# Optimization experiments

Hardware: AMD Instinct MI355X
Metric: run time of the kernel (lower is better)

## Reference

```python
import jax, jax.numpy as jnp
import numpy as np

# ProbAttention (Yangskm/DroneMA-i-), eval mode (dropout=identity).
# Key facts from the source: mask_flag=False, scale=None -> `if self.scale` is
# False, so scores are NOT divided by sqrt(D). The _prob_QK sampling/topk result
# `u` and _get_initial_context are dead code w.r.t. the returned context, so the
# output is exactly dense softmax attention. Inputs are (B, L, H, D); the module
# transposes to (B, H, L, D) and transposes back at the end.

def setup_inputs() -> dict:
    key = jax.random.key(0)
    k1, k2, k3 = jax.random.split(key, 3)
    B, L, H, D = 4, 2048, 8, 64
    return {
        "queries": jax.random.normal(k1, (B, L, H, D), dtype=jnp.float32),
        "keys": jax.random.normal(k2, (B, L, H, D), dtype=jnp.float32),
        "values": jax.random.normal(k3, (B, L, H, D), dtype=jnp.float32),
    }

def reference(queries, keys, values):
    # (B, L, H, D) -> (B, H, L, D)
    q = jnp.swapaxes(queries, 1, 2)
    k = jnp.swapaxes(keys, 1, 2)
    v = jnp.swapaxes(values, 1, 2)
    # dense scores, NO 1/sqrt(D) scaling (scale=None in the original)
    scores = jnp.einsum("bhqd,bhkd->bhqk", q, k)
    attn = jax.nn.softmax(scores, axis=-1)
    ctx = jnp.einsum("bhqk,bhkd->bhqd", attn, v)
    # back to (B, L, H, D)
    return jnp.swapaxes(ctx, 1, 2)
```

## Files before the change

### kernel.cpp

```cpp
#include <hip/hip_runtime.h>
#include <hip/hip_bf16.h>


#define B_ 4
#define L_ 2048
#define H_ 8
#define D_ 64
#define RST_ 512
#define QW_ 32
#define QB_ 128
#define KT_ 64
#define NT_ (L_ / KT_)
#define RS_ 88
#define OTS_ 68
#define SCW_ 35
#define LOG2E_ 1.44269504088896f

#define SMEM_BYTES 35840

typedef _Float16 f16x8 __attribute__((ext_vector_type(8)));
typedef short    s16x4 __attribute__((ext_vector_type(4)));
typedef float    f32x4 __attribute__((ext_vector_type(4)));

__device__ __forceinline__ unsigned pk_bf16(float a, float b) {
    const __bf16 x = (__bf16)a, y = (__bf16)b;
    return ((unsigned)__builtin_bit_cast(unsigned short, y) << 16) |
           (unsigned)__builtin_bit_cast(unsigned short, x);
}

__device__ __forceinline__ f32x4 mfma16_bf16(s16x4 a, s16x4 b, f32x4 c) {
    return __builtin_amdgcn_mfma_f32_16x16x16bf16_1k(a, b, c, 0, 0, 0);
}

__global__ __launch_bounds__(512, 4) void attn_k16pv(
    const float* __restrict__ Qg, const float* __restrict__ Kg,
    const float* __restrict__ Vg, float* __restrict__ Og)
{
    __shared__ __align__(16) char smem[SMEM_BYTES];
    _Float16* Kf = (_Float16*)smem;
    __bf16*   Vt = (__bf16*)(smem + 11264);
    float*    Sc = (float*)smem;

    const int tid  = threadIdx.x;
    const int w    = tid >> 6;
    const int qsub = w & 3;
    const int ks   = w >> 2;
    const int ln   = tid & 15;
    const int lg   = (tid >> 4) & 3;

    const int blk   = (blockIdx.x & 7) * 64 + (blockIdx.x >> 3);
    const int qtile = blk & (L_ / QB_ - 1);
    const int bh    = blk >> 4;
    const int h     = bh & (H_ - 1);
    const int b     = bh >> 3;

    const size_t bhbase = (size_t)b * (L_ * H_ * D_) + (size_t)h * D_;
    const int    qbase  = qtile * QB_ + qsub * QW_;

    f16x8 qf[2][2];
#pragma unroll
    for (int ms = 0; ms < 2; ++ms) {
#pragma unroll
        for (int dc = 0; dc < 2; ++dc) {
            const float* src = Qg + bhbase
                + (size_t)(qbase + ms * 16 + ln) * RST_ + dc * 32 + lg * 8;
            const float4 a = ((const float4*)src)[0];
            const float4 c = ((const float4*)src)[1];
            f16x8 f;
            f[0] = (_Float16)(a.x * LOG2E_); f[1] = (_Float16)(a.y * LOG2E_);
            f[2] = (_Float16)(a.z * LOG2E_); f[3] = (_Float16)(a.w * LOG2E_);
            f[4] = (_Float16)(c.x * LOG2E_); f[5] = (_Float16)(c.y * LOG2E_);
            f[6] = (_Float16)(c.z * LOG2E_); f[7] = (_Float16)(c.w * LOG2E_);
            qf[ms][dc] = f;
        }
    }

    f32x4 o[2][4];
    f32x4 lsum[2];
#pragma unroll
    for (int ms = 0; ms < 2; ++ms) {
        lsum[ms] = (f32x4){0.f, 0.f, 0.f, 0.f};
#pragma unroll
        for (int dg = 0; dg < 4; ++dg) o[ms][dg] = (f32x4){0.f, 0.f, 0.f, 0.f};
    }

    s16x4 ones4;
#pragma unroll
    for (int j = 0; j < 4; ++j) ones4[j] = (short)0x3F80;

    const int krow = tid >> 3;
    const int kd8  = (tid & 7) * 8;
    const int vkp  = (tid & 31) * 2;
    const int vdb  = (tid >> 5) * 4;

    const float* kp  = Kg + bhbase + (size_t)krow * RST_ + kd8;
    const float* vp  = Vg + bhbase + (size_t)vkp * RST_ + vdb;

    float4 kr0, kr1;
    float  vr0[4], vr1[4];

    auto issue = [&]() {
        kr0 = ((const float4*)kp)[0];
        kr1 = ((const float4*)kp)[1];
        const float4 a = ((const float4*)vp)[0];
        const float4 c = ((const float4*)(vp + RST_))[0];
        vr0[0] = a.x; vr0[1] = a.y; vr0[2] = a.z; vr0[3] = a.w;
        vr1[0] = c.x; vr1[1] = c.y; vr1[2] = c.z; vr1[3] = c.w;
        kp += KT_ * RST_;
        vp += KT_ * RST_;
    };
    auto writeKV = [&]() {
        f16x8 kw;
        kw[0] = (_Float16)kr0.x; kw[1] = (_Float16)kr0.y;
        kw[2] = (_Float16)kr0.z; kw[3] = (_Float16)kr0.w;
        kw[4] = (_Float16)kr1.x; kw[5] = (_Float16)kr1.y;
        kw[6] = (_Float16)kr1.z; kw[7] = (_Float16)kr1.w;
        *(f16x8*)&Kf[krow * RS_ + kd8] = kw;
#pragma unroll
        for (int i = 0; i < 4; ++i)
            *(unsigned*)&Vt[(vdb + i) * RS_ + vkp] = pk_bf16(vr0[i], vr1[i]);
    };

    auto compute = [&]() {
        f16x8 kfr[2][2];
#pragma unroll
        for (int dc = 0; dc < 2; ++dc)
#pragma unroll
            for (int kg = 0; kg < 2; ++kg)
                kfr[dc][kg] = *(const f16x8*)
                    &Kf[(ks * 32 + kg * 16 + ln) * RS_ + dc * 32 + lg * 8];
        s16x4 vf[2][4];
#pragma unroll
        for (int kg = 0; kg < 2; ++kg)
#pragma unroll
            for (int dg = 0; dg < 4; ++dg)
                vf[kg][dg] = *(const s16x4*)
                    &Vt[(dg * 16 + ln) * RS_ + ks * 32 + kg * 16 + lg * 4];

#pragma unroll
        for (int ms = 0; ms < 2; ++ms) {
            f32x4 st[2];
#pragma unroll
            for (int kg = 0; kg < 2; ++kg) st[kg] = (f32x4){0.f, 0.f, 0.f, 0.f};
            __builtin_amdgcn_s_setprio(1);
#pragma unroll
            for (int dc = 0; dc < 2; ++dc)
#pragma unroll
                for (int kg = 0; kg < 2; ++kg)
                    st[kg] = __builtin_amdgcn_mfma_f32_16x16x32_f16(
                        kfr[dc][kg], qf[ms][dc], st[kg], 0, 0, 0);
            __builtin_amdgcn_s_setprio(0);

            s16x4 pf[2];
#pragma unroll
            for (int kg = 0; kg < 2; ++kg) {
                const float p0 = __builtin_amdgcn_exp2f(st[kg][0]);
                const float p1 = __builtin_amdgcn_exp2f(st[kg][1]);
                const float p2 = __builtin_amdgcn_exp2f(st[kg][2]);
                const float p3 = __builtin_amdgcn_exp2f(st[kg][3]);
                union { unsigned u[2]; s16x4 v; } pu;
                pu.u[0] = pk_bf16(p0, p1);
                pu.u[1] = pk_bf16(p2, p3);
                pf[kg] = pu.v;
            }

            __builtin_amdgcn_s_setprio(1);
#pragma unroll
            for (int kg = 0; kg < 2; ++kg) {
                lsum[ms] = mfma16_bf16(ones4, pf[kg], lsum[ms]);
#pragma unroll
                for (int dg = 0; dg < 4; ++dg)
                    o[ms][dg] = mfma16_bf16(vf[kg][dg], pf[kg], o[ms][dg]);
            }
            __builtin_amdgcn_s_setprio(0);
        }
    };

    issue();
    for (int t = 0; t < NT_; ++t) {
        __syncthreads();
        writeKV();
        __syncthreads();
        if (t + 1 < NT_) issue();
        compute();
    }

    const int lane = tid & 63;
    __syncthreads();
    if (w >= 4) {
        float* sc = &Sc[((w - 4) * 64 + lane) * SCW_];
#pragma unroll
        for (int ms = 0; ms < 2; ++ms)
#pragma unroll
            for (int dg = 0; dg < 4; ++dg)
#pragma unroll
                for (int r = 0; r < 4; ++r)
                    sc[ms * 16 + dg * 4 + r] = o[ms][dg][r];
        sc[32] = lsum[0][0];
        sc[33] = lsum[1][0];
    }
    __syncthreads();
    if (w < 4) {
        const float* sc = &Sc[(w * 64 + lane) * SCW_];
        float po[2][4][4];
#pragma unroll
        for (int ms = 0; ms < 2; ++ms)
#pragma unroll
            for (int dg = 0; dg < 4; ++dg)
#pragma unroll
                for (int r = 0; r < 4; ++r)
                    po[ms][dg][r] = o[ms][dg][r] + sc[ms * 16 + dg * 4 + r];
        const float linv[2] = {1.0f / (lsum[0][0] + sc[32]),
                               1.0f / (lsum[1][0] + sc[33])};

        float* Ot = (float*)(smem + w * 8960);
        const int qr = lane >> 2;
        const int ch = lane & 3;
#pragma unroll
        for (int ms = 0; ms < 2; ++ms) {
#pragma unroll
            for (int dg = 0; dg < 4; ++dg) {
#pragma unroll
                for (int i = 0; i < 2; ++i) {
                    float2 pr;
                    pr.x = po[ms][dg][2 * i]     * linv[ms];
                    pr.y = po[ms][dg][2 * i + 1] * linv[ms];
                    *(float2*)&Ot[ln * OTS_ + dg * 16 + lg * 4 + 2 * i] = pr;
                }
            }
#pragma unroll
            for (int p = 0; p < 4; ++p) {
                const float4 vo = *(const float4*)&Ot[qr * OTS_ + ch * 4 + p * 16];
                *(float4*)(Og + bhbase
                    + (size_t)(qbase + ms * 16 + qr) * RST_ + ch * 4 + p * 16) = vo;
            }
        }
    }
}

extern "C" void kernel_launch(void* const* d_in, const int* in_sizes, int n_in,
                              void* d_out, int out_size, void* d_ws, size_t ws_size,
                              hipStream_t stream) {
    const float* Q = (const float*)d_in[0];
    const float* K = (const float*)d_in[1];
    const float* V = (const float*)d_in[2];
    float* O = (float*)d_out;

    const int grid = B_ * H_ * (L_ / QB_);
    attn_k16pv<<<grid, 512, 0, stream>>>(Q, K, V, O);
}
```

Measured before the change: 64.20 us.

## Double-buffer K/V shared tiles and widen V fragment reads

Splits the K and V shared-memory tiles into two buffers so each iteration writes the next tile while computing on the current one. This halves the barriers per tile and keeps two global loads in flight. V columns are also permuted when stored, so each lane loads one 8-element vector in place of two 4-element reads. In exchange, shared memory grows from about 35KB to 45KB, and more staged registers are held, which may reduce occupancy.

```diff
diff --git a/kernel.cpp b/kernel.cpp
--- a/kernel.cpp
+++ b/kernel.cpp
@@ -16,10 +16,11 @@
 #define SCW_ 35
 #define LOG2E_ 1.44269504088896f
 
-#define SMEM_BYTES 35840
+#define SMEM_BYTES 45056
 
 typedef _Float16 f16x8 __attribute__((ext_vector_type(8)));
 typedef short    s16x4 __attribute__((ext_vector_type(4)));
+typedef short    s16x8 __attribute__((ext_vector_type(8)));
 typedef float    f32x4 __attribute__((ext_vector_type(4)));
 
 __device__ __forceinline__ unsigned pk_bf16(float a, float b) {
@@ -32,14 +33,18 @@
     return __builtin_amdgcn_mfma_f32_16x16x16bf16_1k(a, b, c, 0, 0, 0);
 }
 
-__global__ __launch_bounds__(512, 4) void attn_k16pv(
+struct Stage { float4 k0, k1, v0, v1; };
+
+__global__ __launch_bounds__(512, 4) void attn_dbuf1b(
     const float* __restrict__ Qg, const float* __restrict__ Kg,
     const float* __restrict__ Vg, float* __restrict__ Og)
 {
     __shared__ __align__(16) char smem[SMEM_BYTES];
-    _Float16* Kf = (_Float16*)smem;
-    __bf16*   Vt = (__bf16*)(smem + 11264);
-    float*    Sc = (float*)smem;
+    _Float16* Kf0 = (_Float16*)smem;
+    _Float16* Kf1 = (_Float16*)(smem + 11264);
+    __bf16*   Vt0 = (__bf16*)(smem + 22528);
+    __bf16*   Vt1 = (__bf16*)(smem + 33792);
+    float*    Sc  = (float*)smem;
 
     const int tid  = threadIdx.x;
     const int w    = tid >> 6;
@@ -92,51 +97,52 @@
     const int kd8  = (tid & 7) * 8;
     const int vkp  = (tid & 31) * 2;
     const int vdb  = (tid >> 5) * 4;
-
-    const float* kp  = Kg + bhbase + (size_t)krow * RST_ + kd8;
-    const float* vp  = Vg + bhbase + (size_t)vkp * RST_ + vdb;
-
-    float4 kr0, kr1;
-    float  vr0[4], vr1[4];
-
-    auto issue = [&]() {
-        kr0 = ((const float4*)kp)[0];
-        kr1 = ((const float4*)kp)[1];
-        const float4 a = ((const float4*)vp)[0];
-        const float4 c = ((const float4*)(vp + RST_))[0];
-        vr0[0] = a.x; vr0[1] = a.y; vr0[2] = a.z; vr0[3] = a.w;
-        vr1[0] = c.x; vr1[1] = c.y; vr1[2] = c.z; vr1[3] = c.w;
-        kp += KT_ * RST_;
-        vp += KT_ * RST_;
-    };
-    auto writeKV = [&]() {
+    const int vpos = (vkp & 32) + (((vkp & 15) >> 2) * 8) + (((vkp >> 4) & 1) * 4) + (vkp & 3);
+
+    const float* kpA = Kg + bhbase + (size_t)krow * RST_ + kd8;
+    const float* vpA = Vg + bhbase + (size_t)vkp * RST_ + vdb;
+    const float* kpB = kpA + (size_t)KT_ * RST_;
+    const float* vpB = vpA + (size_t)KT_ * RST_;
+
+    Stage sA, sB;
+
+    auto issueS = [&](Stage& s, const float*& kp, const float*& vp) {
+        s.k0 = ((const float4*)kp)[0];
+        s.k1 = ((const float4*)kp)[1];
+        s.v0 = ((const float4*)vp)[0];
+        s.v1 = ((const float4*)(vp + RST_))[0];
+        kp += (size_t)2 * KT_ * RST_;
+        vp += (size_t)2 * KT_ * RST_;
+    };
+    auto writeKV = [&](_Float16* Kf, __bf16* Vt, const Stage& s) {
         f16x8 kw;
-        kw[0] = (_Float16)kr0.x; kw[1] = (_Float16)kr0.y;
-        kw[2] = (_Float16)kr0.z; kw[3] = (_Float16)kr0.w;
-        kw[4] = (_Float16)kr1.x; kw[5] = (_Float16)kr1.y;
-        kw[6] = (_Float16)kr1.z; kw[7] = (_Float16)kr1.w;
+        kw[0] = (_Float16)s.k0.x; kw[1] = (_Float16)s.k0.y;
+        kw[2] = (_Float16)s.k0.z; kw[3] = (_Float16)s.k0.w;
+        kw[4] = (_Float16)s.k1.x; kw[5] = (_Float16)s.k1.y;
+        kw[6] = (_Float16)s.k1.z; kw[7] = (_Float16)s.k1.w;
         *(f16x8*)&Kf[krow * RS_ + kd8] = kw;
+        const float av[4] = {s.v0.x, s.v0.y, s.v0.z, s.v0.w};
+        const float bv[4] = {s.v1.x, s.v1.y, s.v1.z, s.v1.w};
 #pragma unroll
         for (int i = 0; i < 4; ++i)
-            *(unsigned*)&Vt[(vdb + i) * RS_ + vkp] = pk_bf16(vr0[i], vr1[i]);
-    };
-
-    auto compute = [&]() {
-        f16x8 kfr[2][2];
+            *(unsigned*)&Vt[(vdb + i) * RS_ + vpos] = pk_bf16(av[i], bv[i]);
+    };
+
+    f16x8 kfr[2][2];
+    s16x8 vfp[4];
+    auto readFrags = [&](const _Float16* Kf, const __bf16* Vt) {
 #pragma unroll
         for (int dc = 0; dc < 2; ++dc)
 #pragma unroll
             for (int kg = 0; kg < 2; ++kg)
                 kfr[dc][kg] = *(const f16x8*)
                     &Kf[(ks * 32 + kg * 16 + ln) * RS_ + dc * 32 + lg * 8];
-        s16x4 vf[2][4];
-#pragma unroll
-        for (int kg = 0; kg < 2; ++kg)
-#pragma unroll
-            for (int dg = 0; dg < 4; ++dg)
-                vf[kg][dg] = *(const s16x4*)
-                    &Vt[(dg * 16 + ln) * RS_ + ks * 32 + kg * 16 + lg * 4];
-
+#pragma unroll
+        for (int dg = 0; dg < 4; ++dg)
+            vfp[dg] = *(const s16x8*)&Vt[(dg * 16 + ln) * RS_ + ks * 32 + lg * 8];
+    };
+
+    auto computeT = [&]() {
 #pragma unroll
         for (int ms = 0; ms < 2; ++ms) {
             f32x4 st[2];
@@ -169,24 +175,37 @@
             for (int kg = 0; kg < 2; ++kg) {
                 lsum[ms] = mfma16_bf16(ones4, pf[kg], lsum[ms]);
 #pragma unroll
-                for (int dg = 0; dg < 4; ++dg)
-                    o[ms][dg] = mfma16_bf16(vf[kg][dg], pf[kg], o[ms][dg]);
+                for (int dg = 0; dg < 4; ++dg) {
+                    const s16x4 vh = (kg == 0)
+                        ? __builtin_shufflevector(vfp[dg], vfp[dg], 0, 1, 2, 3)
+                        : __builtin_shufflevector(vfp[dg], vfp[dg], 4, 5, 6, 7);
+                    o[ms][dg] = mfma16_bf16(vh, pf[kg], o[ms][dg]);
+                }
             }
             __builtin_amdgcn_s_setprio(0);
         }
     };
 
-    issue();
-    for (int t = 0; t < NT_; ++t) {
+    issueS(sA, kpA, vpA);
+    issueS(sB, kpB, vpB);
+    writeKV(Kf0, Vt0, sA);
+    issueS(sA, kpA, vpA);
+    __syncthreads();
+
+    for (int t = 0; t < NT_; t += 2) {
+        readFrags(Kf0, Vt0);
+        writeKV(Kf1, Vt1, sB);
+        if (t + 3 < NT_) issueS(sB, kpB, vpB);
+        computeT();
         __syncthreads();
-        writeKV();
+        readFrags(Kf1, Vt1);
+        if (t + 2 < NT_) writeKV(Kf0, Vt0, sA);
+        if (t + 4 < NT_) issueS(sA, kpA, vpA);
+        computeT();
         __syncthreads();
-        if (t + 1 < NT_) issue();
-        compute();
     }
 
     const int lane = tid & 63;
-    __syncthreads();
     if (w >= 4) {
         float* sc = &Sc[((w - 4) * 64 + lane) * SCW_];
 #pragma unroll
@@ -247,5 +266,5 @@
     float* O = (float*)d_out;
 
     const int grid = B_ * H_ * (L_ / QB_);
-    attn_k16pv<<<grid, 512, 0, stream>>>(Q, K, V, O);
-}
+    attn_dbuf1b<<<grid, 512, 0, stream>>>(Q, K, V, O);
+}
```

New measurement: 112.7 us. +75.5%, slower.
